# Optimization experiments

Hardware: AMD Instinct MI355X
Metric: run time of the kernel (lower is better)

The kernel has to match this reference:

```python
import jax, jax.numpy as jnp
import numpy as np

C = 1024        # number of classes
N = 8           # proxies per class
ALLNUM = C * N  # 8192 total proxies
DIM = 512
R = 0.05
TOPK = int(np.ceil(R * ALLNUM))  # 410
LAM = 0.3
B = 2048


def setup_inputs() -> dict:
    key = jax.random.key(0)
    k1, k2, k3 = jax.random.split(key, 3)
    inp = jax.random.normal(k1, (B, DIM), dtype=jnp.float32)
    target = jax.random.randint(k2, (B,), 0, C, dtype=jnp.int64)
    # kaiming-uniform-initialized proxies approximated by scaled normal init
    proxies = jax.random.normal(k3, (DIM, ALLNUM), dtype=jnp.float32)
    instance_label = jnp.repeat(jnp.arange(C, dtype=jnp.int64), N)  # [ALLNUM]
    return {"input": inp, "target": target, "Proxies": proxies,
            "instance_label": instance_label}


def reference(input, target, Proxies, instance_label):
    # L2-normalize each proxy column (F.normalize along dim=0, eps=1e-12)
    norm = jnp.maximum(jnp.linalg.norm(Proxies, axis=0, keepdims=True), 1e-12)
    centers = Proxies / norm                             # [DIM, ALLNUM]
    similarity = input @ centers                          # [B, ALLNUM]

    positive_mask = (target[:, None] == instance_label[None, :]).astype(similarity.dtype)
    _, indices = jax.lax.top_k(similarity + 1000.0 * positive_mask, TOPK)  # [B, TOPK]

    rows = jnp.arange(similarity.shape[0])[:, None]
    mask = jnp.zeros_like(similarity).at[rows, indices].set(1.0)
    prob_a = mask * similarity                            # sparse-masked similarities

    y_instance_onehot = jax.nn.one_hot(instance_label, C, dtype=similarity.dtype)  # [ALLNUM, C]
    logits = prob_a @ y_instance_onehot                   # [B, C]

    y_target_onehot = jax.nn.one_hot(target, C, dtype=similarity.dtype)  # [B, C]
    logits_mask = 1.0 - (logits == 0.0).astype(similarity.dtype)

    # scale_mask_softmax with scale=1 along dim=1
    e = jnp.exp(logits) * logits_mask
    predict = e / (1e-8 + jnp.sum(e, axis=1, keepdims=True))
    lossClassify = jnp.mean(jnp.sum(-y_target_onehot * jnp.log(predict + 1e-20), axis=1))

    # proxy regularizer: cross-entropy of proxy-vs-class logits
    simCenter = centers.T @ centers                       # [ALLNUM, ALLNUM]
    centers_logits = simCenter @ y_instance_onehot        # [ALLNUM, C]
    logp = jax.nn.log_softmax(centers_logits, axis=1)
    reg = -jnp.mean(jnp.take_along_axis(logp, instance_label[:, None], axis=1))

    return (lossClassify + LAM * reg, lossClassify)
```

## Files before the change

### kernel.cpp

```cpp
#include <hip/hip_runtime.h>
#include <hip/hip_bf16.h>
#include <math.h>

#define C_CLS   1024
#define NPROXY  8
#define ALLNUM  8192
#define DIM     512
#define TOPK    410
#define LAM     0.3f
#define BATCH   2048

#define BAND_CAP_BLK 40
#define ROW_CAP      512
#define GCAP         64

typedef __bf16 bf16x8 __attribute__((ext_vector_type(8)));
typedef float floatx4 __attribute__((ext_vector_type(4)));
typedef unsigned short ushort_t;

#define WS_RNORM 0
#define WS_SIG   8192
#define WS_LP    10240
#define WS_RP    12288
#define WS_CNT   14336
#define WS_NDEF  16384
#define WS_FLAG  18432
#define WS_CLS   20480
#define WS_BVAL  (WS_CLS + 2048*1024)
#define WS_BCOL  (WS_BVAL + 2048*512)
#define WS_ABF   (WS_BCOL + 2048*256)
#define WS_PBF   (WS_ABF + 524288)
#define WS_STBF  (WS_PBF + 2097152)
#define WS_LOG   (WS_STBF + 262144)

__device__ inline float block_reduce(float v, int is_max, float* red, int t) {
    #pragma unroll
    for (int o = 32; o > 0; o >>= 1) {
        float w = __shfl_down(v, o);
        v = is_max ? fmaxf(v, w) : (v + w);
    }
    __syncthreads();
    if ((t & 63) == 0) red[t >> 6] = v;
    __syncthreads();
    return is_max ? fmaxf(fmaxf(red[0], red[1]), fmaxf(red[2], red[3]))
                  : (red[0] + red[1] + red[2] + red[3]);
}

__device__ inline ushort_t f2bf(float f) {
    unsigned u = __float_as_uint(f);
    return (ushort_t)((u + 0x7FFFu + ((u >> 16) & 1u)) >> 16);
}

__device__ inline float bf2f(ushort_t u) {
    return __uint_as_float(((unsigned)u) << 16);
}

__device__ inline void ld_g2l_16(const void* g, void* l) {
    __builtin_amdgcn_global_load_lds(
        (const __attribute__((address_space(1))) unsigned int*)g,
        (__attribute__((address_space(3))) unsigned int*)l,
        16, 0, 0);
}

__device__ inline unsigned f2ord(float f) {
    unsigned u = __float_as_uint(f);
    return (u & 0x80000000u) ? ~u : (u | 0x80000000u);
}

__global__ __launch_bounds__(256) void k_prep1(const float* __restrict__ P,
                                               const float* __restrict__ input,
                                               float* __restrict__ rnorm,
                                               float* __restrict__ rowsig,
                                               ushort_t* __restrict__ Abf,
                                               ushort_t* __restrict__ Pbf,
                                               ushort_t* __restrict__ Stbf,
                                               unsigned* __restrict__ zaux) {
    __shared__ float tile[32][33];
    __shared__ float s_rn[32];
    float* cred = &tile[0][0];
    int bx = blockIdx.x, t = threadIdx.x;
    if (bx < 256) {
        int tc = t & 31, g = t >> 5;
        int c = bx * 32 + tc;
        const float* pc = P + (size_t)(g * 64) * ALLNUM + c;
        float s = 0.f;
        #pragma unroll 8
        for (int d = 0; d < 64; ++d) {
            float v = pc[(size_t)d * ALLNUM];
            s += v * v;
        }
        cred[g * 32 + tc] = s;
        __syncthreads();
        if (g == 0) {
            float tot = 0.f;
            #pragma unroll
            for (int k = 0; k < 8; ++k) tot += cred[k * 32 + tc];
            float r = 1.0f / fmaxf(sqrtf(tot), 1e-12f);
            rnorm[c] = r;
            s_rn[tc] = r;
        }
        __syncthreads();
        #pragma unroll
        for (int p = 0; p < 8; ++p) {
            int idx = t + 256 * p;
            int d = idx >> 2, cc = idx & 3;
            const float* pp = P + (size_t)d * ALLNUM + bx * 32 + cc * 8;
            const float* rr = &s_rn[cc * 8];
            float4 a = *(const float4*)pp;
            float4 b = *(const float4*)(pp + 4);
            float v = a.x * rr[0] + a.y * rr[1] + a.z * rr[2] + a.w * rr[3] +
                      b.x * rr[4] + b.y * rr[5] + b.z * rr[6] + b.w * rr[7];
            Stbf[(size_t)(bx * 4 + cc) * DIM + d] = f2bf(v);
        }
    } else if (bx < 256 + 1024) {
        int a = bx - 256;
        int idx = a * 256 + t;
        float4 v = ((const float4*)input)[idx];
        ushort4 o;
        o.x = f2bf(v.x); o.y = f2bf(v.y); o.z = f2bf(v.z); o.w = f2bf(v.w);
        ((ushort4*)Abf)[idx] = o;
        float sq = v.x * v.x + v.y * v.y + v.z * v.z + v.w * v.w;
        #pragma unroll
        for (int off = 32; off > 0; off >>= 1) sq += __shfl_down(sq, off);
        int lane = t & 63, w = t >> 6;
        if (lane == 0) cred[w] = sq;
        __syncthreads();
        if (t == 0) {
            rowsig[2 * a]     = sqrtf(cred[0] + cred[1]);
            rowsig[2 * a + 1] = sqrtf(cred[2] + cred[3]);
        }
    } else if (bx < 256 + 1024 + 4096) {
        int id = bx - 1280;
        int c0 = (id & 255) * 32, r0 = (id >> 8) * 32;
        int tc = t & 31, tr = t >> 5;
        #pragma unroll
        for (int p = 0; p < 4; ++p)
            tile[tr + p * 8][tc] = P[(size_t)(r0 + tr + p * 8) * ALLNUM + c0 + tc];
        __syncthreads();
        #pragma unroll
        for (int p = 0; p < 4; ++p) {
            int oc = tr + p * 8;
            Pbf[(size_t)(c0 + oc) * DIM + r0 + tc] = f2bf(tile[tc][oc]);
        }
    } else {
        for (int i = t; i < 3 * 2048; i += 256) zaux[i] = 0u;
    }
}

__global__ __launch_bounds__(512, 2) void k_gemms(const ushort_t* __restrict__ Abf,
                                                  const ushort_t* __restrict__ Pbf,
                                                  const ushort_t* __restrict__ Stbf,
                                                  const float* __restrict__ rnorm,
                                                  const float* __restrict__ rowsig,
                                                  const int* __restrict__ target,
                                                  float* __restrict__ g_cls,
                                                  float* __restrict__ g_bval,
                                                  ushort_t* __restrict__ g_bcol,
                                                  unsigned* __restrict__ g_cnt,
                                                  unsigned* __restrict__ g_ndef,
                                                  unsigned* __restrict__ g_flag,
                                                  ushort_t* __restrict__ logits) {
    __shared__ __align__(16) ushort_t smem[65536];
    int bx = blockIdx.x, t = threadIdx.x;
    int w = t >> 6, lane = t & 63;
    int ml = lane & 15, q4 = lane >> 4;
    int wm = w >> 2, wn = w & 3;

    int isg0 = (bx < 256);
    const ushort_t* Ap;
    const ushort_t* Bp;
    int bi, bj;
    if (isg0) {
        int x_ = bx & 7, r_ = bx >> 3;
        bi = (r_ >> 2) * 256;
        bj = (x_ * 4 + (r_ & 3)) * 256;
        Ap = Abf; Bp = Pbf;
    } else {
        int id = bx - 256;
        bi = (id >> 2) * 256;
        bj = (id & 3) * 256;
        Ap = Pbf; Bp = Stbf;
    }

    floatx4 acc[8][4];
    #pragma unroll
    for (int mf = 0; mf < 8; ++mf)
        #pragma unroll
        for (int nf = 0; nf < 4; ++nf)
            acc[mf][nf] = (floatx4){0.f, 0.f, 0.f, 0.f};

    #define STAGE_HALF(Mp, rbase, k0, dstoff) do {                             \
        _Pragma("unroll")                                                      \
        for (int it_ = 0; it_ < 2; ++it_) {                                    \
            int c_ = (it_ * 8 + w) * 64 + lane;                                \
            int m_ = c_ >> 3, s_ = c_ & 7, q_ = s_ ^ (m_ & 7);                 \
            ld_g2l_16((Mp) + ((size_t)((rbase) + m_) << 9) + (k0) + q_ * 8,    \
                      &smem[(dstoff) + c_ * 8]);                               \
        } } while (0)

    STAGE_HALF(Ap, bi,       0, 0);
    STAGE_HALF(Ap, bi + 128, 0, 8192);
    STAGE_HALF(Bp, bj,       0, 16384);
    STAGE_HALF(Bp, bj + 128, 0, 24576);
    asm volatile("s_waitcnt vmcnt(0)" ::: "memory");
    __builtin_amdgcn_s_barrier();
    asm volatile("" ::: "memory");

    bf16x8 bfr[2][4];
    #pragma unroll
    for (int tt = 0; tt < 8; ++tt) {
        const int Xo = (tt & 1) ? 32768 : 0;
        const int Yo = 32768 - Xo;
        const ushort_t* Xa = &smem[Xo];
        const ushort_t* Xb = &smem[Xo + 16384];
        #pragma unroll
        for (int p = 0; p < 4; ++p) {
            if (tt < 7) {
                if (p == 0) STAGE_HALF(Ap, bi,       (tt + 1) * 64, Yo);
                if (p == 1) STAGE_HALF(Ap, bi + 128, (tt + 1) * 64, Yo + 8192);
                if (p == 2) STAGE_HALF(Bp, bj,       (tt + 1) * 64, Yo + 16384);
                if (p == 3) STAGE_HALF(Bp, bj + 128, (tt + 1) * 64, Yo + 24576);
            }
            if (p == 0) {
                #pragma unroll
                for (int kk = 0; kk < 2; ++kk)
                    #pragma unroll
                    for (int nf = 0; nf < 4; ++nf) {
                        int n = wn * 64 + nf * 16 + ml;
                        int s = (kk * 4 + q4) ^ (n & 7);
                        bfr[kk][nf] = *(const bf16x8*)&Xb[n * 64 + s * 8];
                    }
            }
            bf16x8 af[2][2];
            #pragma unroll
            for (int kk = 0; kk < 2; ++kk)
                #pragma unroll
                for (int mi = 0; mi < 2; ++mi) {
                    int m = wm * 128 + (p * 2 + mi) * 16 + ml;
                    int s = (kk * 4 + q4) ^ (m & 7);
                    af[kk][mi] = *(const bf16x8*)&Xa[m * 64 + s * 8];
                }
            __builtin_amdgcn_s_setprio(1);
            #pragma unroll
            for (int kk = 0; kk < 2; ++kk)
                #pragma unroll
                for (int mi = 0; mi < 2; ++mi)
                    #pragma unroll
                    for (int nf = 0; nf < 4; ++nf)
                        acc[p * 2 + mi][nf] = __builtin_amdgcn_mfma_f32_16x16x32_bf16(
                            af[kk][mi], bfr[kk][nf], acc[p * 2 + mi][nf], 0, 0, 0);
            __builtin_amdgcn_s_setprio(0);
            if (p == 3) asm volatile("s_waitcnt vmcnt(0)" ::: "memory");
            __builtin_amdgcn_s_barrier();
            if (p == 3) asm volatile("" ::: "memory");
        }
    }
    #undef STAGE_HALF

    if (isg0) {
        unsigned char* sb8 = (unsigned char*)smem;
        float*    e_cls = (float*)sb8;
        float*    e_bv  = (float*)(sb8 + 32768);
        ushort_t* e_bc  = (ushort_t*)(sb8 + 73728);
        unsigned* e_cnt = (unsigned*)(sb8 + 94208);
        unsigned* e_nd  = (unsigned*)(sb8 + 95232);

        #pragma unroll
        for (int i = t; i < 8192; i += 512) e_cls[i] = 0.f;
        if (t < 256) { e_cnt[t] = 0u; e_nd[t] = 0u; }
        __syncthreads();

        #pragma unroll
        for (int mf = 0; mf < 8; ++mf) {
            int rl0 = wm * 128 + mf * 16 + q4 * 4;
            int rowb = bi + rl0;
            float4 rs4 = *(const float4*)&rowsig[rowb];
            int4   tg4 = *(const int4*)&target[rowb];
            #pragma unroll
            for (int nf = 0; nf < 4; ++nf) {
                int cl = wn * 64 + nf * 16 + ml;
                int col = bj + cl;
                float sc = rnorm[col];
                int cls = col >> 3;
                int clsl = cl >> 3;
                #pragma unroll
                for (int i = 0; i < 4; ++i) {
                    int rl = rl0 + i;
                    float v = acc[mf][nf][i] * sc;
                    float sg = ((const float*)&rs4)[i] * (1.0f / 22.616f);
                    float hiT = 1.80f * sg, loT = 1.47f * sg;
                    int tg = ((const int*)&tg4)[i];
                    if (cls == tg) {
                        atomicAdd(&e_cls[rl * 32 + clsl], v);
                    } else if (v >= hiT) {
                        atomicAdd(&e_cls[rl * 32 + clsl], v);
                        atomicAdd(&e_nd[rl], 1u);
                    } else if (v >= loT) {
                        unsigned u = atomicAdd(&e_cnt[rl], 1u);
                        if (u < BAND_CAP_BLK) {
                            e_bv[rl * BAND_CAP_BLK + u] = v;
                            e_bc[rl * BAND_CAP_BLK + u] = (ushort_t)col;
                        }
                    }
                }
            }
        }
        __syncthreads();

        int bjc = bj >> 3;
        #pragma unroll
        for (int i = t; i < 8192; i += 512) {
            int rl = i >> 5, c = i & 31;
            g_cls[(size_t)(bi + rl) * C_CLS + bjc + c] = e_cls[i];
        }
        if (t < 256) {
            int row = bi + t;
            unsigned cbb = e_cnt[t];
            unsigned nd = e_nd[t];
            if (nd) atomicAdd(&g_ndef[row], nd);
            if (cbb) {
                unsigned cc = (cbb > BAND_CAP_BLK) ? BAND_CAP_BLK : cbb;
                unsigned base = atomicAdd(&g_cnt[row], cc);
                if (cbb > BAND_CAP_BLK || base + cc > ROW_CAP) g_flag[row] = 1u;
                for (unsigned j = 0; j < cc; ++j) {
                    if (base + j >= ROW_CAP) break;
                    g_bval[(size_t)row * ROW_CAP + base + j] = e_bv[t * BAND_CAP_BLK + j];
                    g_bcol[(size_t)row * ROW_CAP + base + j] = e_bc[t * BAND_CAP_BLK + j];
                }
            }
        }
    } else {
        #pragma unroll
        for (int mf = 0; mf < 8; ++mf) {
            int rowb = bi + wm * 128 + mf * 16 + q4 * 4;
            float4 rnr = *(const float4*)&rnorm[rowb];
            #pragma unroll
            for (int nf = 0; nf < 4; ++nf) {
                int col = bj + wn * 64 + nf * 16 + ml;
                #pragma unroll
                for (int i = 0; i < 4; ++i)
                    logits[(size_t)(rowb + i) * C_CLS + col] =
                        f2bf(acc[mf][nf][i] * ((const float*)&rnr)[i]);
            }
        }
    }
}

__device__ inline void suffix_select1(unsigned* s_hist, unsigned kk,
                                      unsigned* s_wtot, unsigned* sh_bin,
                                      unsigned* sh_k, int t, int lane, int wid) {
    unsigned h = s_hist[t];
    unsigned v = h;
    #pragma unroll
    for (int off = 1; off < 64; off <<= 1) {
        unsigned o = __shfl_down(v, off);
        if (lane + off < 64) v += o;
    }
    if (lane == 0) s_wtot[wid] = v;
    __syncthreads();
    unsigned above = v - h;
    for (int w2 = wid + 1; w2 < 4; ++w2) above += s_wtot[w2];
    unsigned cum = above + h;
    if (cum >= kk && above < kk) { *sh_bin = (unsigned)t; *sh_k = kk - above; }
    __syncthreads();
}

__global__ __launch_bounds__(256) void k_finish(const int* __restrict__ target,
                                                const float* __restrict__ rowsig,
                                                const float* __restrict__ rnorm,
                                                const ushort_t* __restrict__ Abf,
                                                const ushort_t* __restrict__ Pbf,
                                                const float* __restrict__ g_cls,
                                                const float* __restrict__ g_bval,
                                                const ushort_t* __restrict__ g_bcol,
                                                const unsigned* __restrict__ g_cnt,
                                                const unsigned* __restrict__ g_ndef,
                                                const unsigned* __restrict__ g_flag,
                                                float* __restrict__ loss_part,
                                                const ushort_t* __restrict__ logits,
                                                float* __restrict__ reg_part) {
    __shared__ __align__(16) unsigned char smem[16384];
    int bx = blockIdx.x, t = threadIdx.x;
    int lane = t & 63, wid = t >> 6;

    if (bx < 2048) {
        float*    s_cls  = (float*)smem;
        float*    s_bval = (float*)(smem + 4096);
        ushort_t* s_bcol = (ushort_t*)(smem + 6144);
        unsigned* s_hist = (unsigned*)(smem + 7168);
        float*    s_arow = (float*)(smem + 8192);
        unsigned* s_wtot = (unsigned*)(smem + 10240);
        unsigned* shv    = (unsigned*)(smem + 10256);
        float*    shf    = (float*)(smem + 10272);
        float*    red    = (float*)(smem + 10288);
        float*    s_gval = (float*)(smem + 10304);

        int b = bx;
        int tgt = target[b];
        float sig = rowsig[b] * (1.0f / 22.616f);
        float hiT = 1.80f * sig, loT = 1.47f * sig;
        float binscale = 256.0f / (hiT - loT);

        ((float4*)s_cls)[t] = ((const float4*)(g_cls + (size_t)b * C_CLS))[t];
        unsigned cnt = g_cnt[b], nd = g_ndef[b], fl = g_flag[b];
        int kq = (TOPK - NPROXY) - (int)nd;
        int ok = (fl == 0u) && (cnt <= ROW_CAP) && (kq >= 0) && ((int)cnt >= kq);
        if (t == 0) shv[1] = 0u;
        s_hist[t] = 0u;
        __syncthreads();

        if (ok) {
            if (kq > 0) {
                for (int j = t; j < (int)cnt; j += 256) {
                    float v = g_bval[(size_t)b * ROW_CAP + j];
                    s_bval[j] = v;
                    s_bcol[j] = g_bcol[(size_t)b * ROW_CAP + j];
                    int bin = (int)((v - loT) * binscale);
                    bin = (bin > 255) ? 255 : bin;
                    atomicAdd(&s_hist[bin], 1u);
                }
                __syncthreads();
                suffix_select1(s_hist, (unsigned)kq, s_wtot, &shv[2], &shv[3], t, lane, wid);
                int Bb = (int)shv[2];
                int knew = (int)shv[3];
                for (int j = t; j < (int)cnt; j += 256) {
                    float v = s_bval[j];
                    int bin = (int)((v - loT) * binscale);
                    bin = (bin > 255) ? 255 : bin;
                    if (bin == Bb) {
                        unsigned g = atomicAdd(&shv[1], 1u);
                        if (g < GCAP) s_gval[g] = v;
                    }
                }
                __syncthreads();
                int gc = (int)shv[1];
                if (gc <= GCAP) {
                    if (t < gc) {
                        float vj = s_gval[t];
                        unsigned g = 0, geq = 0;
                        for (int i = 0; i < gc; ++i) {
                            float vi = s_gval[i];
                            g   += (vi > vj) ? 1u : 0u;
                            geq += (vi >= vj) ? 1u : 0u;
                        }
                        if (g < (unsigned)knew && geq >= (unsigned)knew) shf[0] = vj;
                    }
                } else {
                    for (int j = t; j < (int)cnt; j += 256) {
                        float vj = s_bval[j];
                        unsigned g = 0, geq = 0;
                        for (int i = 0; i < (int)cnt; ++i) {
                            float vi = s_bval[i];
                            g   += (vi > vj) ? 1u : 0u;
                            geq += (vi >= vj) ? 1u : 0u;
                        }
                        if (g < (unsigned)kq && geq >= (unsigned)kq) shf[0] = vj;
                    }
                }
                __syncthreads();
                float thr = shf[0];
                for (int j = t; j < (int)cnt; j += 256)
                    if (s_bval[j] >= thr)
                        atomicAdd(&s_cls[s_bcol[j] >> 3], s_bval[j]);
            }
        } else {
            for (int i = t; i < DIM; i += 256)
                s_arow[i] = bf2f(Abf[(size_t)b * DIM + i]);
            #pragma unroll
            for (int i = 0; i < 4; ++i) s_cls[t + 256 * i] = 0.f;
            __syncthreads();
            float4 v4[8];
            for (int p = 0; p < 8; ++p) {
                int f = t + 256 * p;
                float vv[4];
                for (int e = 0; e < 4; ++e) {
                    int col = 4 * f + e;
                    const ushort_t* pc = Pbf + (size_t)col * DIM;
                    float a = 0.f;
                    for (int d = 0; d < DIM; ++d)
                        a += s_arow[d] * bf2f(pc[d]);
                    vv[e] = a * rnorm[col];
                }
                float4 o; o.x = vv[0]; o.y = vv[1]; o.z = vv[2]; o.w = vv[3];
                v4[p] = o;
            }
            #pragma unroll
            for (int p = 0; p < 8; ++p) {
                int f = t + 256 * p;
                const float* pv = (const float*)&v4[p];
                if ((f >> 1) == tgt)
                    atomicAdd(&s_cls[tgt], pv[0] + pv[1] + pv[2] + pv[3]);
            }
            unsigned L = 0u, R = 0xFFFFFFFFu;
            for (int it = 0; it < 33 && R - L > 1; ++it) {
                unsigned mid = L + ((R - L) >> 1);
                float c = 0.f;
                #pragma unroll
                for (int p = 0; p < 8; ++p) {
                    int f = t + 256 * p;
                    const float* pv = (const float*)&v4[p];
                    if ((f >> 1) != tgt) {
                        #pragma unroll
                        for (int e = 0; e < 4; ++e)
                            c += (f2ord(pv[e]) >= mid) ? 1.f : 0.f;
                    }
                }
                c = block_reduce(c, 0, red, t);
                if (c >= (float)(TOPK - NPROXY)) L = mid; else R = mid;
                __syncthreads();
            }
            #pragma unroll
            for (int p = 0; p < 8; ++p) {
                int f = t + 256 * p;
                const float* pv = (const float*)&v4[p];
                if ((f >> 1) != tgt) {
                    #pragma unroll
                    for (int e = 0; e < 4; ++e)
                        if (f2ord(pv[e]) >= L)
                            atomicAdd(&s_cls[f >> 1], pv[e]);
                }
            }
        }
        __syncthreads();

        float4 cv = ((const float4*)s_cls)[t];
        float m = -1e30f;
        if (cv.x != 0.0f) m = fmaxf(m, cv.x);
        if (cv.y != 0.0f) m = fmaxf(m, cv.y);
        if (cv.z != 0.0f) m = fmaxf(m, cv.z);
        if (cv.w != 0.0f) m = fmaxf(m, cv.w);
        m = block_reduce(m, 1, red, t);
        float se = 0.f;
        if (cv.x != 0.0f) se += expf(cv.x - m);
        if (cv.y != 0.0f) se += expf(cv.y - m);
        if (cv.z != 0.0f) se += expf(cv.z - m);
        if (cv.w != 0.0f) se += expf(cv.w - m);
        se = block_reduce(se, 0, red, t);
        if (t == 0) {
            float lt = s_cls[tgt];
            float predict_t = expf(lt - m) / (1e-8f * expf(-m) + se);
            loss_part[b] = -logf(predict_t + 1e-20f);
        }
    } else {
        __shared__ float bsum[4];
        int rb = bx - 2048;
        int i = rb * 4 + wid;
        const ushort_t* row = logits + (size_t)i * C_CLS;
        uint4 c0 = ((const uint4*)row)[lane];
        uint4 c1 = ((const uint4*)(row + 512))[lane];

        float f[16];
        const unsigned* u0 = (const unsigned*)&c0;
        const unsigned* u1 = (const unsigned*)&c1;
        #pragma unroll
        for (int k = 0; k < 4; ++k) {
            f[2 * k]     = __uint_as_float(u0[k] << 16);
            f[2 * k + 1] = __uint_as_float(u0[k] & 0xFFFF0000u);
            f[8 + 2 * k]     = __uint_as_float(u1[k] << 16);
            f[8 + 2 * k + 1] = __uint_as_float(u1[k] & 0xFFFF0000u);
        }

        int cstar = i >> 3;
        int chunk = cstar >> 9, within = cstar & 511;
        float sd = 0.f;
        if (lane == (within >> 3)) sd = f[chunk * 8 + (within & 7)];

        float m = -1e30f;
        #pragma unroll
        for (int k = 0; k < 16; ++k) m = fmaxf(m, f[k]);
        #pragma unroll
        for (int off = 32; off > 0; off >>= 1) m = fmaxf(m, __shfl_xor(m, off));

        float se = 0.f;
        #pragma unroll
        for (int k = 0; k < 16; ++k) se += expf(f[k] - m);
        #pragma unroll
        for (int off = 32; off > 0; off >>= 1) se += __shfl_xor(se, off);
        #pragma unroll
        for (int off = 32; off > 0; off >>= 1) sd += __shfl_xor(sd, off);

        if (lane == 0) bsum[wid] = m + logf(se) - sd;
        __syncthreads();
        if (t == 0)
            reg_part[rb] = bsum[0] + bsum[1] + bsum[2] + bsum[3];
    }
}

__global__ __launch_bounds__(256) void k_final(const float* __restrict__ lp,
                                               const float* __restrict__ rp,
                                               float* __restrict__ out) {
    __shared__ float red[4];
    int t = threadIdx.x;
    float4 a = ((const float4*)lp)[t];
    float4 b = ((const float4*)lp)[t + 256];
    float4 c = ((const float4*)rp)[t];
    float4 d = ((const float4*)rp)[t + 256];
    float ls = a.x + a.y + a.z + a.w + b.x + b.y + b.z + b.w;
    float rs = c.x + c.y + c.z + c.w + d.x + d.y + d.z + d.w;
    ls = block_reduce(ls, 0, red, t);
    rs = block_reduce(rs, 0, red, t);
    if (t == 0) {
        float lc = ls / (float)BATCH;
        float rg = rs / (float)ALLNUM;
        out[0] = lc + LAM * rg;
        out[1] = lc;
    }
}

extern "C" void kernel_launch(void* const* d_in, const int* in_sizes, int n_in,
                              void* d_out, int out_size, void* d_ws, size_t ws_size,
                              hipStream_t stream) {
    const float* input  = (const float*)d_in[0];
    const int*   target = (const int*)d_in[1];
    const float* P      = (const float*)d_in[2];

    float* ws        = (float*)d_ws;
    float* rnorm     = ws + WS_RNORM;
    float* rowsig    = ws + WS_SIG;
    float* loss_part = ws + WS_LP;
    float* reg_part  = ws + WS_RP;
    unsigned* g_cnt  = (unsigned*)(ws + WS_CNT);
    unsigned* g_ndef = (unsigned*)(ws + WS_NDEF);
    unsigned* g_flag = (unsigned*)(ws + WS_FLAG);
    float* g_cls     = ws + WS_CLS;
    float* g_bval    = ws + WS_BVAL;
    ushort_t* g_bcol = (ushort_t*)(ws + WS_BCOL);
    ushort_t* Abf    = (ushort_t*)(ws + WS_ABF);
    ushort_t* Pbf    = (ushort_t*)(ws + WS_PBF);
    ushort_t* Stbf   = (ushort_t*)(ws + WS_STBF);
    ushort_t* logits = (ushort_t*)(ws + WS_LOG);
    float* out       = (float*)d_out;

    hipLaunchKernelGGL(k_prep1, dim3(256 + 1024 + 4096 + 1), dim3(256), 0, stream,
                       P, input, rnorm, rowsig, Abf, Pbf, Stbf, g_cnt);
    hipLaunchKernelGGL(k_gemms, dim3(384), dim3(512), 0, stream,
                       Abf, Pbf, Stbf, rnorm, rowsig, target,
                       g_cls, g_bval, g_bcol, g_cnt, g_ndef, g_flag, logits);
    hipLaunchKernelGGL(k_finish, dim3(4096), dim3(256), 0, stream,
                       target, rowsig, rnorm, Abf, Pbf,
                       g_cls, g_bval, g_bcol, g_cnt, g_ndef, g_flag,
                       loss_part, logits, reg_part);
    hipLaunchKernelGGL(k_final, dim3(1), dim3(256), 0, stream,
                       loss_part, reg_part, out);
}
```

Measured before the change: 152.7 us.

## Halve GEMM tile width, triple-buffer K stages, and remap blocks across XCDs

The fused GEMM kernel moves from 256x256 to 256x128 output tiles, doubling the grid to 768 blocks so the 256 compute units are covered more evenly. The K loop becomes a three-stage LDS ring with two stages prefetched, using a partial vmcnt wait and a single barrier per step in place of the per-quarter barriers. The block id is remapped with a stride-8 interleave, which looks meant to spread work across the chiplets and improve L2 locality. The per-block band capacity is lowered to match the narrower tile, which may raise overflow flags more often, and the larger LDS footprint cuts occupancy to one block per CU.

Measured after the change: 155.6 us. Within noise of the previous version (+1.9%).

```diff
diff --git a/kernel.cpp b/kernel.cpp
--- a/kernel.cpp
+++ b/kernel.cpp
@@ -10,7 +10,7 @@
 #define LAM     0.3f
 #define BATCH   2048
 
-#define BAND_CAP_BLK 40
+#define BAND_CAP_BLK 28
 #define ROW_CAP      512
 #define GCAP         64
 
@@ -147,7 +147,7 @@
     }
 }
 
-__global__ __launch_bounds__(512, 2) void k_gemms(const ushort_t* __restrict__ Abf,
+__global__ __launch_bounds__(512, 1) void k_gemms(const ushort_t* __restrict__ Abf,
                                                   const ushort_t* __restrict__ Pbf,
                                                   const ushort_t* __restrict__ Stbf,
                                                   const float* __restrict__ rnorm,
@@ -160,119 +160,110 @@
                                                   unsigned* __restrict__ g_ndef,
                                                   unsigned* __restrict__ g_flag,
                                                   ushort_t* __restrict__ logits) {
-    __shared__ __align__(16) ushort_t smem[65536];
+    __shared__ __align__(16) ushort_t smem[73728];
     int bx = blockIdx.x, t = threadIdx.x;
     int w = t >> 6, lane = t & 63;
     int ml = lane & 15, q4 = lane >> 4;
-    int wm = w >> 2, wn = w & 3;
-
-    int isg0 = (bx < 256);
+    int wm = w >> 1, wn = w & 1;
+
+    int wid = (bx & 7) * 96 + (bx >> 3);
+    int isg0 = (wid < 512);
     const ushort_t* Ap;
     const ushort_t* Bp;
     int bi, bj;
     if (isg0) {
-        int x_ = bx & 7, r_ = bx >> 3;
-        bi = (r_ >> 2) * 256;
-        bj = (x_ * 4 + (r_ & 3)) * 256;
+        bi = (wid & 7) * 256;
+        bj = (wid >> 3) * 128;
         Ap = Abf; Bp = Pbf;
     } else {
-        int id = bx - 256;
-        bi = (id >> 2) * 256;
-        bj = (id & 3) * 256;
+        int id1 = wid - 512;
+        bi = (id1 & 31) * 256;
+        bj = (id1 >> 5) * 128;
         Ap = Pbf; Bp = Stbf;
     }
 
-    floatx4 acc[8][4];
+    floatx4 acc[4][4];
     #pragma unroll
-    for (int mf = 0; mf < 8; ++mf)
+    for (int mf = 0; mf < 4; ++mf)
         #pragma unroll
         for (int nf = 0; nf < 4; ++nf)
             acc[mf][nf] = (floatx4){0.f, 0.f, 0.f, 0.f};
 
-    #define STAGE_HALF(Mp, rbase, k0, dstoff) do {                             \
+    #define STAGE(t_, k0_) do {                                                \
+        int bo_ = ((t_) % 3) * 24576;                                          \
+        _Pragma("unroll")                                                      \
+        for (int it_ = 0; it_ < 4; ++it_) {                                    \
+            int c_ = w * 256 + it_ * 64 + lane;                                \
+            int m_ = c_ >> 3, q_ = (c_ & 7) ^ (m_ & 7);                        \
+            ld_g2l_16(Ap + ((size_t)(bi + m_) << 9) + (k0_) + q_ * 8,          \
+                      &smem[bo_ + c_ * 8]);                                    \
+        }                                                                      \
         _Pragma("unroll")                                                      \
         for (int it_ = 0; it_ < 2; ++it_) {                                    \
-            int c_ = (it_ * 8 + w) * 64 + lane;                                \
-            int m_ = c_ >> 3, s_ = c_ & 7, q_ = s_ ^ (m_ & 7);                 \
-            ld_g2l_16((Mp) + ((size_t)((rbase) + m_) << 9) + (k0) + q_ * 8,    \
-                      &smem[(dstoff) + c_ * 8]);                               \
+            int c_ = w * 128 + it_ * 64 + lane;                                \
+            int m_ = c_ >> 3, q_ = (c_ & 7) ^ (m_ & 7);                        \
+            ld_g2l_16(Bp + ((size_t)(bj + m_) << 9) + (k0_) + q_ * 8,          \
+                      &smem[bo_ + 16384 + c_ * 8]);                            \
         } } while (0)
 
-    STAGE_HALF(Ap, bi,       0, 0);
-    STAGE_HALF(Ap, bi + 128, 0, 8192);
-    STAGE_HALF(Bp, bj,       0, 16384);
-    STAGE_HALF(Bp, bj + 128, 0, 24576);
-    asm volatile("s_waitcnt vmcnt(0)" ::: "memory");
-    __builtin_amdgcn_s_barrier();
-    asm volatile("" ::: "memory");
-
-    bf16x8 bfr[2][4];
+    STAGE(0, 0);
+    STAGE(1, 64);
+
     #pragma unroll
     for (int tt = 0; tt < 8; ++tt) {
-        const int Xo = (tt & 1) ? 32768 : 0;
-        const int Yo = 32768 - Xo;
-        const ushort_t* Xa = &smem[Xo];
-        const ushort_t* Xb = &smem[Xo + 16384];
-        #pragma unroll
-        for (int p = 0; p < 4; ++p) {
-            if (tt < 7) {
-                if (p == 0) STAGE_HALF(Ap, bi,       (tt + 1) * 64, Yo);
-                if (p == 1) STAGE_HALF(Ap, bi + 128, (tt + 1) * 64, Yo + 8192);
-                if (p == 2) STAGE_HALF(Bp, bj,       (tt + 1) * 64, Yo + 16384);
-                if (p == 3) STAGE_HALF(Bp, bj + 128, (tt + 1) * 64, Yo + 24576);
-            }
-            if (p == 0) {
+        if (tt < 7) asm volatile("s_waitcnt vmcnt(6)" ::: "memory");
+        else        asm volatile("s_waitcnt vmcnt(0)" ::: "memory");
+        __builtin_amdgcn_s_barrier();
+        if (tt < 6) STAGE(tt + 2, (tt + 2) * 64);
+
+        const ushort_t* Xa = &smem[(tt % 3) * 24576];
+        const ushort_t* Xb = Xa + 16384;
+        bf16x8 af[2][4], bfr[2][4];
+        #pragma unroll
+        for (int kk = 0; kk < 2; ++kk) {
+            #pragma unroll
+            for (int nf = 0; nf < 4; ++nf) {
+                int n = wn * 64 + nf * 16 + ml;
+                int s = (kk * 4 + q4) ^ (n & 7);
+                bfr[kk][nf] = *(const bf16x8*)&Xb[n * 64 + s * 8];
+            }
+            #pragma unroll
+            for (int mf = 0; mf < 4; ++mf) {
+                int m = wm * 64 + mf * 16 + ml;
+                int s = (kk * 4 + q4) ^ (m & 7);
+                af[kk][mf] = *(const bf16x8*)&Xa[m * 64 + s * 8];
+            }
+        }
+        __builtin_amdgcn_s_setprio(1);
+        #pragma unroll
+        for (int kk = 0; kk < 2; ++kk)
+            #pragma unroll
+            for (int mf = 0; mf < 4; ++mf)
                 #pragma unroll
-                for (int kk = 0; kk < 2; ++kk)
-                    #pragma unroll
-                    for (int nf = 0; nf < 4; ++nf) {
-                        int n = wn * 64 + nf * 16 + ml;
-                        int s = (kk * 4 + q4) ^ (n & 7);
-                        bfr[kk][nf] = *(const bf16x8*)&Xb[n * 64 + s * 8];
-                    }
-            }
-            bf16x8 af[2][2];
-            #pragma unroll
-            for (int kk = 0; kk < 2; ++kk)
-                #pragma unroll
-                for (int mi = 0; mi < 2; ++mi) {
-                    int m = wm * 128 + (p * 2 + mi) * 16 + ml;
-                    int s = (kk * 4 + q4) ^ (m & 7);
-                    af[kk][mi] = *(const bf16x8*)&Xa[m * 64 + s * 8];
-                }
-            __builtin_amdgcn_s_setprio(1);
-            #pragma unroll
-            for (int kk = 0; kk < 2; ++kk)
-                #pragma unroll
-                for (int mi = 0; mi < 2; ++mi)
-                    #pragma unroll
-                    for (int nf = 0; nf < 4; ++nf)
-                        acc[p * 2 + mi][nf] = __builtin_amdgcn_mfma_f32_16x16x32_bf16(
-                            af[kk][mi], bfr[kk][nf], acc[p * 2 + mi][nf], 0, 0, 0);
-            __builtin_amdgcn_s_setprio(0);
-            if (p == 3) asm volatile("s_waitcnt vmcnt(0)" ::: "memory");
-            __builtin_amdgcn_s_barrier();
-            if (p == 3) asm volatile("" ::: "memory");
-        }
-    }
-    #undef STAGE_HALF
+                for (int nf = 0; nf < 4; ++nf)
+                    acc[mf][nf] = __builtin_amdgcn_mfma_f32_16x16x32_bf16(
+                        af[kk][mf], bfr[kk][nf], acc[mf][nf], 0, 0, 0);
+        __builtin_amdgcn_s_setprio(0);
+    }
+    #undef STAGE
+    __syncthreads();
 
     if (isg0) {
         unsigned char* sb8 = (unsigned char*)smem;
         float*    e_cls = (float*)sb8;
-        float*    e_bv  = (float*)(sb8 + 32768);
-        ushort_t* e_bc  = (ushort_t*)(sb8 + 73728);
-        unsigned* e_cnt = (unsigned*)(sb8 + 94208);
-        unsigned* e_nd  = (unsigned*)(sb8 + 95232);
-
-        #pragma unroll
-        for (int i = t; i < 8192; i += 512) e_cls[i] = 0.f;
+        float*    e_bv  = (float*)(sb8 + 16384);
+        ushort_t* e_bc  = (ushort_t*)(sb8 + 45056);
+        unsigned* e_cnt = (unsigned*)(sb8 + 59392);
+        unsigned* e_nd  = (unsigned*)(sb8 + 60416);
+
+        #pragma unroll
+        for (int i = t; i < 4096; i += 512) e_cls[i] = 0.f;
         if (t < 256) { e_cnt[t] = 0u; e_nd[t] = 0u; }
         __syncthreads();
 
         #pragma unroll
-        for (int mf = 0; mf < 8; ++mf) {
-            int rl0 = wm * 128 + mf * 16 + q4 * 4;
+        for (int mf = 0; mf < 4; ++mf) {
+            int rl0 = wm * 64 + mf * 16 + q4 * 4;
             int rowb = bi + rl0;
             float4 rs4 = *(const float4*)&rowsig[rowb];
             int4   tg4 = *(const int4*)&target[rowb];
@@ -291,9 +282,9 @@
                     float hiT = 1.80f * sg, loT = 1.47f * sg;
                     int tg = ((const int*)&tg4)[i];
                     if (cls == tg) {
-                        atomicAdd(&e_cls[rl * 32 + clsl], v);
+                        atomicAdd(&e_cls[rl * 16 + clsl], v);
                     } else if (v >= hiT) {
-                        atomicAdd(&e_cls[rl * 32 + clsl], v);
+                        atomicAdd(&e_cls[rl * 16 + clsl], v);
                         atomicAdd(&e_nd[rl], 1u);
                     } else if (v >= loT) {
                         unsigned u = atomicAdd(&e_cnt[rl], 1u);
@@ -309,8 +300,8 @@
 
         int bjc = bj >> 3;
         #pragma unroll
-        for (int i = t; i < 8192; i += 512) {
-            int rl = i >> 5, c = i & 31;
+        for (int i = t; i < 4096; i += 512) {
+            int rl = i >> 4, c = i & 15;
             g_cls[(size_t)(bi + rl) * C_CLS + bjc + c] = e_cls[i];
         }
         if (t < 256) {
@@ -331,8 +322,8 @@
         }
     } else {
         #pragma unroll
-        for (int mf = 0; mf < 8; ++mf) {
-            int rowb = bi + wm * 128 + mf * 16 + q4 * 4;
+        for (int mf = 0; mf < 4; ++mf) {
+            int rowb = bi + wm * 64 + mf * 16 + q4 * 4;
             float4 rnr = *(const float4*)&rnorm[rowb];
             #pragma unroll
             for (int nf = 0; nf < 4; ++nf) {
@@ -633,7 +624,7 @@
 
     hipLaunchKernelGGL(k_prep1, dim3(256 + 1024 + 4096 + 1), dim3(256), 0, stream,
                        P, input, rnorm, rowsig, Abf, Pbf, Stbf, g_cnt);
-    hipLaunchKernelGGL(k_gemms, dim3(384), dim3(512), 0, stream,
+    hipLaunchKernelGGL(k_gemms, dim3(768), dim3(512), 0, stream,
                        Abf, Pbf, Stbf, rnorm, rowsig, target,
                        g_cls, g_bval, g_bcol, g_cnt, g_ndef, g_flag, logits);
     hipLaunchKernelGGL(k_finish, dim3(4096), dim3(256), 0, stream,
```
